# Kernel optimization log

Hardware: AMD Instinct MI355X
Metric: run time of the kernel (lower is better)

Reference implementation:

```python
import jax, jax.numpy as jnp
import numpy as np

B, L, C, R = 2, 1024, 64, 32
RV, DQK, H, NSINK = 32, 64, 8, 4


def setup_inputs() -> dict:
    key = jax.random.key(0)
    ks = jax.random.split(key, 10)
    s_in = 1.0 / np.sqrt(C * R)
    s_r = 1.0 / np.sqrt(R)
    s_rv = 1.0 / np.sqrt(RV)
    return {
        "x": jax.random.normal(ks[0], (B, L, C, R), jnp.float32),
        "Wq": jax.random.normal(ks[1], (C * R, H * DQK), jnp.float32) * s_in,
        "bq": jax.random.normal(ks[2], (H * DQK,), jnp.float32) * s_in,
        "Wk": jax.random.normal(ks[3], (C * R, DQK), jnp.float32) * s_in,
        "bk": jax.random.normal(ks[4], (DQK,), jnp.float32) * s_in,
        "Wv": jax.random.normal(ks[5], (C, R, RV), jnp.float32) * s_r,
        "bv": jax.random.normal(ks[6], (C, RV), jnp.float32) * s_r,
        "Wo": jax.random.normal(ks[7], (C, RV, R), jnp.float32) * s_rv,
        "bo": jax.random.normal(ks[8], (C, R), jnp.float32) * s_rv,
        "sink_q": jax.random.normal(ks[9], (H, NSINK, DQK), jnp.float32),
    }


def reference(x, Wq, bq, Wk, bk, Wv, bv, Wo, bo, sink_q):
    b, l, c, r = x.shape
    h, d_qk = H, DQK
    scale = 1.0 / np.sqrt(d_qk)

    x_flat = x.reshape(b, l, c * r)
    q = (x_flat @ Wq + bq).reshape(b, l, h, d_qk)          # (B,L,H,D)
    k = x_flat @ Wk + bk                                    # (B,L,D) shared MQA key

    # fp32 softmax over time, as in the original
    logits = (jnp.einsum('blhd,bsd->bhls', q, k).astype(jnp.float32) * scale)
    attn = jax.nn.softmax(logits, axis=-1).astype(x.dtype)  # (B,H,L,S)

    # per-channel value projection (B,L,C,RV)
    v = jnp.einsum('blcr,cro->blco', x, Wv) + bv

    # AV with extra channel axis, fused with head-mean (same math as
    # einsum('bhls,bscv->bhlcv').mean(1))
    y = jnp.einsum('bhls,bscv->blcv', attn, v) / h          # (B,L,C,RV)

    # sink-query branch: learned queries attend over time, mean over (H, S)
    logits_s = (jnp.einsum('hsd,bld->bhsl', sink_q, k).astype(jnp.float32) * scale)
    attn_s = jax.nn.softmax(logits_s, axis=-1).astype(x.dtype)  # (B,H,S,L)
    y_sink = jnp.einsum('bhsl,blcv->bcv', attn_s, v) / (h * NSINK)
    y = y + y_sink[:, None]                                 # broadcast over L

    # per-channel output projection + residual
    y = jnp.einsum('blcv,cvr->blcr', y, Wo) + bo
    return x + y
```

## Files before the change

kernel.cpp:

```cpp
#include <hip/hip_runtime.h>
#include <hip/hip_bf16.h>
#include <math.h>


typedef __attribute__((ext_vector_type(8))) short short8;
typedef __attribute__((ext_vector_type(4))) short short4v;
typedef __attribute__((ext_vector_type(4))) float float4v;

__device__ __forceinline__ short f2b(float f) {
    __hip_bfloat16 h = __float2bfloat16(f);
    return __builtin_bit_cast(short, h);
}
__device__ __forceinline__ float b2f(short s) {
    unsigned u = ((unsigned)(unsigned short)s) << 16;
    return __builtin_bit_cast(float, u);
}

__global__ __launch_bounds__(256) void convert_w_kernel(
    const float* __restrict__ Wq, const float* __restrict__ Wk,
    short* __restrict__ Wt)
{
    const int n0 = blockIdx.x * 64;
    const int k0 = blockIdx.y * 64;
    const int tid = threadIdx.x;
    __shared__ float ts[64][65];
    for (int i = tid; i < 4096; i += 256) {
        int kk = i >> 6, nn = i & 63;
        int n = n0 + nn, k = k0 + kk;
        float v = (n < 512) ? Wq[(long)k * 512 + n] : Wk[(long)k * 64 + (n - 512)];
        ts[kk][nn] = v;
    }
    __syncthreads();
    for (int i = tid; i < 4096; i += 256) {
        int nn = i >> 6, kk = i & 63;
        Wt[(long)(n0 + nn) * 2048 + k0 + kk] = f2b(ts[kk][nn]);
    }
}

__global__ __launch_bounds__(256) void vproj_kernel(
    const float* __restrict__ x, const float* __restrict__ Wv,
    const float* __restrict__ bv, short* __restrict__ vt,
    short* __restrict__ xb)
{
    const int c = blockIdx.x;
    const int chunk = blockIdx.y;
    const int b = chunk >> 4;
    const int l0 = (chunk & 15) * 64;
    const int tid = threadIdx.x;
    __shared__ float Wc[32][33];
    __shared__ float xs[64][33];
    for (int i = tid; i < 1024; i += 256)
        Wc[i >> 5][i & 31] = Wv[(c * 32 + (i >> 5)) * 32 + (i & 31)];
    for (int i = tid; i < 2048; i += 256) {
        int s = i >> 5, r = i & 31;
        long gi = ((long)(b << 10) + l0 + s) * 2048 + c * 32 + r;
        float v = x[gi];
        xs[s][r] = v;
        xb[gi] = f2b(v);
    }
    __syncthreads();
    const int s = tid & 63;
    const int og = tid >> 6;
    #pragma unroll
    for (int oi = 0; oi < 8; ++oi) {
        int o = og * 8 + oi;
        float acc = bv[c * 32 + o];
        #pragma unroll
        for (int r = 0; r < 32; ++r) acc += xs[s][r] * Wc[r][o];
        vt[(long)b * (2048 * 1024) + (long)(c * 32 + o) * 1024 + l0 + s] = f2b(acc);
    }
}

__global__ __launch_bounds__(256) void qkproj_kernel(
    const short* __restrict__ xb, const short* __restrict__ Wt,
    float* __restrict__ qkpart)
{
    __shared__ short As[64][72];
    __shared__ short Bs[64][72];

    const int tid = threadIdx.x;
    const int wave = tid >> 6;
    const int lane = tid & 63;
    const int wm = wave >> 1, wn = wave & 1;
    const int m15 = lane & 15;
    const int quad = lane >> 4;
    const int row0 = blockIdx.y * 64;
    const int col0 = blockIdx.x * 64;
    const int kbase = blockIdx.z * 1024;
    float* outz = qkpart + (long)blockIdx.z * 1179648;

    float4v acc[2][2];
    #pragma unroll
    for (int i = 0; i < 2; ++i)
        #pragma unroll
        for (int j = 0; j < 2; ++j)
            #pragma unroll
            for (int r = 0; r < 4; ++r) acc[i][j][r] = 0.f;

    for (int kt = 0; kt < 16; ++kt) {
        int k0 = kbase + kt * 64;
        #pragma unroll
        for (int p = 0; p < 2; ++p) {
            int i = tid + p * 256;
            int m = i >> 3, kq = i & 7;
            *reinterpret_cast<short8*>(&As[m][kq * 8]) =
                *reinterpret_cast<const short8*>(&xb[(long)(row0 + m) * 2048 + k0 + kq * 8]);
        }
        #pragma unroll
        for (int p = 0; p < 2; ++p) {
            int i = tid + p * 256;
            int n = i >> 3, kq = i & 7;
            *reinterpret_cast<short8*>(&Bs[n][kq * 8]) =
                *reinterpret_cast<const short8*>(&Wt[(long)(col0 + n) * 2048 + k0 + kq * 8]);
        }
        __syncthreads();
        #pragma unroll
        for (int ks = 0; ks < 2; ++ks) {
            short8 a[2], b[2];
            #pragma unroll
            for (int t = 0; t < 2; ++t) {
                a[t] = *reinterpret_cast<const short8*>(&As[wm * 32 + t * 16 + m15][ks * 32 + quad * 8]);
                b[t] = *reinterpret_cast<const short8*>(&Bs[wn * 32 + t * 16 + m15][ks * 32 + quad * 8]);
            }
            #pragma unroll
            for (int ti = 0; ti < 2; ++ti)
                #pragma unroll
                for (int tj = 0; tj < 2; ++tj)
                    acc[ti][tj] = __builtin_amdgcn_mfma_f32_16x16x32_bf16(
                        a[ti], b[tj], acc[ti][tj], 0, 0, 0);
        }
        __syncthreads();
    }

    #pragma unroll
    for (int ti = 0; ti < 2; ++ti)
        #pragma unroll
        for (int r = 0; r < 4; ++r) {
            int row = row0 + wm * 32 + ti * 16 + quad * 4 + r;
            #pragma unroll
            for (int tj = 0; tj < 2; ++tj) {
                int col = col0 + wn * 32 + tj * 16 + m15;
                outz[(long)row * 576 + col] = acc[ti][tj][r];
            }
        }
}

__global__ __launch_bounds__(256) void convert_qk_kernel(
    const float* __restrict__ qkpart, const float* __restrict__ bq,
    const float* __restrict__ bk, short* __restrict__ qkb)
{
    int id = blockIdx.x * 256 + threadIdx.x;
    float4 a = reinterpret_cast<const float4*>(qkpart)[id];
    float4 b = reinterpret_cast<const float4*>(qkpart + 1179648)[id];
    int col4 = (id % 144) * 4;
    float4 bias = (col4 < 512)
        ? *reinterpret_cast<const float4*>(&bq[col4])
        : *reinterpret_cast<const float4*>(&bk[col4 - 512]);
    short4v o;
    o[0] = f2b(a.x + b.x + bias.x);
    o[1] = f2b(a.y + b.y + bias.y);
    o[2] = f2b(a.z + b.z + bias.z);
    o[3] = f2b(a.w + b.w + bias.w);
    reinterpret_cast<short4v*>(qkb)[id] = o;
}

__global__ __launch_bounds__(256) void qk_s_kernel(
    const short* __restrict__ qkb, short* __restrict__ S)
{
    const int s0 = blockIdx.x * 64;
    const int l0 = blockIdx.y * 64;
    const int b = blockIdx.z;
    const int tid = threadIdx.x;
    short* Sz = S + ((long)b << 23);

    __shared__ short Qs[64][520];
    __shared__ short Ks[64][72];

    #pragma unroll
    for (int p = 0; p < 16; ++p) {
        int i = tid + p * 256;
        int row = i >> 6, d8 = i & 63;
        *reinterpret_cast<short8*>(&Qs[row][d8 * 8]) =
            *reinterpret_cast<const short8*>(&qkb[(long)((b << 10) + l0 + row) * 576 + d8 * 8]);
    }
    #pragma unroll
    for (int p = 0; p < 2; ++p) {
        int i = tid + p * 256;
        int row = i >> 3, d8 = i & 7;
        *reinterpret_cast<short8*>(&Ks[row][d8 * 8]) =
            *reinterpret_cast<const short8*>(&qkb[(long)((b << 10) + s0 + row) * 576 + 512 + d8 * 8]);
    }
    __syncthreads();

    const int wave = tid >> 6;
    const int lane = tid & 63;
    const int wm = wave >> 1, wn = wave & 1;
    const int m15 = lane & 15;
    const int quad = lane >> 4;

    for (int h = 0; h < 8; ++h) {
        float4v acc[2][2];
        #pragma unroll
        for (int i = 0; i < 2; ++i)
            #pragma unroll
            for (int j = 0; j < 2; ++j)
                #pragma unroll
                for (int r = 0; r < 4; ++r) acc[i][j][r] = 0.f;

        #pragma unroll
        for (int ks = 0; ks < 2; ++ks) {
            short8 a[2], bfr[2];
            #pragma unroll
            for (int t = 0; t < 2; ++t) {
                a[t]   = *reinterpret_cast<const short8*>(
                    &Qs[wm * 32 + t * 16 + m15][h * 64 + ks * 32 + quad * 8]);
                bfr[t] = *reinterpret_cast<const short8*>(
                    &Ks[wn * 32 + t * 16 + m15][ks * 32 + quad * 8]);
            }
            #pragma unroll
            for (int ti = 0; ti < 2; ++ti)
                #pragma unroll
                for (int tj = 0; tj < 2; ++tj)
                    acc[ti][tj] = __builtin_amdgcn_mfma_f32_16x16x32_bf16(
                        a[ti], bfr[tj], acc[ti][tj], 0, 0, 0);
        }

        #pragma unroll
        for (int ti = 0; ti < 2; ++ti)
            #pragma unroll
            for (int r = 0; r < 4; ++r) {
                int l = l0 + wm * 32 + ti * 16 + quad * 4 + r;
                #pragma unroll
                for (int tj = 0; tj < 2; ++tj) {
                    int s = s0 + wn * 32 + tj * 16 + m15;
                    Sz[((long)h << 20) + (l << 10) + s] = f2b(acc[ti][tj][r] * 0.125f);
                }
            }
    }
}

__global__ __launch_bounds__(256) void softmax_avg_kernel(
    const short* __restrict__ S, short* __restrict__ P)
{
    const int l = blockIdx.x;
    const int b = blockIdx.y;
    const int tid = threadIdx.x;
    const int h = tid >> 5, j = tid & 31;
    const short* Sz = S + ((long)b << 23);

    __shared__ float es[8][1032];
    __shared__ float invd[8];

    const short* row = &Sz[((long)h << 20) + (l << 10)];
    float vals[32];
    float pm = -1e30f;
    #pragma unroll
    for (int i = 0; i < 32; ++i) {
        float f = b2f(row[i * 32 + j]);
        vals[i] = f;
        pm = fmaxf(pm, f);
    }
    #pragma unroll
    for (int off = 16; off > 0; off >>= 1) pm = fmaxf(pm, __shfl_down(pm, off, 32));
    pm = __shfl(pm, 0, 32);

    float ps = 0.f;
    #pragma unroll
    for (int i = 0; i < 32; ++i) {
        float e = __expf(vals[i] - pm);
        vals[i] = e;
        ps += e;
    }
    #pragma unroll
    for (int off = 16; off > 0; off >>= 1) ps += __shfl_down(ps, off, 32);
    if (j == 0) invd[h] = 1.f / (8.f * ps);
    __syncthreads();

    const float w = invd[h];
    #pragma unroll
    for (int i = 0; i < 32; ++i) es[h][i * 32 + j] = vals[i] * w;
    __syncthreads();

    for (int s = tid; s < 1024; s += 256) {
        float p = 0.f;
        #pragma unroll
        for (int hh = 0; hh < 8; ++hh) p += es[hh][s];
        P[((long)b << 20) + (l << 10) + s] = f2b(p);
    }
}

__global__ __launch_bounds__(256) void sink_kernel(
    const float* __restrict__ sink_q, const short* __restrict__ qkb,
    float* __restrict__ Psink)
{
    const int z = blockIdx.x;
    const int b = z >> 5;
    const int idx = z & 31;
    const int tid = threadIdx.x;

    __shared__ float sq[64];
    __shared__ float lgl[1024];
    __shared__ float red[4];
    __shared__ float mxs, invs;

    if (tid < 64) sq[tid] = sink_q[idx * 64 + tid];
    __syncthreads();

    float lmax = -1e30f;
    for (int l = tid; l < 1024; l += 256) {
        const short* kp = &qkb[(long)((b << 10) + l) * 576 + 512];
        float acc = 0.f;
        #pragma unroll
        for (int d8 = 0; d8 < 8; ++d8) {
            short8 kv = *reinterpret_cast<const short8*>(&kp[d8 * 8]);
            #pragma unroll
            for (int j = 0; j < 8; ++j) acc += b2f(kv[j]) * sq[d8 * 8 + j];
        }
        acc *= 0.125f;
        lgl[l] = acc;
        lmax = fmaxf(lmax, acc);
    }
    #pragma unroll
    for (int off = 32; off > 0; off >>= 1) lmax = fmaxf(lmax, __shfl_down(lmax, off, 64));
    if ((tid & 63) == 0) red[tid >> 6] = lmax;
    __syncthreads();
    if (tid == 0) mxs = fmaxf(fmaxf(red[0], red[1]), fmaxf(red[2], red[3]));
    __syncthreads();

    const float m = mxs;
    float psum = 0.f;
    for (int l = tid; l < 1024; l += 256) {
        float e = __expf(lgl[l] - m);
        lgl[l] = e;
        psum += e;
    }
    #pragma unroll
    for (int off = 32; off > 0; off >>= 1) psum += __shfl_down(psum, off, 64);
    if ((tid & 63) == 0) red[tid >> 6] = psum;
    __syncthreads();
    if (tid == 0) invs = 1.f / (red[0] + red[1] + red[2] + red[3]);
    __syncthreads();

    const float wgt = invs * (1.f / 32.f);
    for (int l = tid; l < 1024; l += 256)
        atomicAdd(&Psink[(b << 10) + l], lgl[l] * wgt);
}

__global__ __launch_bounds__(256) void sinky_kernel(
    const float* __restrict__ Psink, const short* __restrict__ vt,
    float* __restrict__ Ysink)
{
    const int b = blockIdx.y;
    const int tid = threadIdx.x;
    __shared__ float ps[1024];
    {
        float4 v = reinterpret_cast<const float4*>(&Psink[b << 10])[tid];
        *reinterpret_cast<float4*>(&ps[tid * 4]) = v;
    }
    __syncthreads();
    const int wave = tid >> 6;
    const int lane = tid & 63;
    const int co = blockIdx.x * 4 + wave;
    const short* vp = &vt[((long)b * 2048 + co) * 1024];
    float acc = 0.f;
    #pragma unroll
    for (int t = 0; t < 16; ++t) {
        int l = t * 64 + lane;
        acc += ps[l] * b2f(vp[l]);
    }
    #pragma unroll
    for (int off = 32; off > 0; off >>= 1) acc += __shfl_down(acc, off, 64);
    if (lane == 0) Ysink[(b << 11) + co] = acc;
}

__global__ __launch_bounds__(256) void y_fused_kernel(
    const short* __restrict__ P, const short* __restrict__ vt,
    const float* __restrict__ Ysink, const float* __restrict__ Wo,
    const float* __restrict__ bo, const float* __restrict__ x,
    float* __restrict__ out)
{
    __shared__ short As[128][72];
    __shared__ short Bs[64][72];

    const int tid = threadIdx.x;
    const int b = blockIdx.z;
    const int col0 = blockIdx.x * 64;
    const int row0 = blockIdx.y * 128;
    const short* Pz = P + ((long)b << 20);
    const short* Vz = vt + ((long)b * 2048 * 1024);

    const int wave = tid >> 6;
    const int lane = tid & 63;
    const int wm = wave >> 1, wn = wave & 1;
    const int m15 = lane & 15;
    const int quad = lane >> 4;

    float4v acc[4][2];
    #pragma unroll
    for (int i = 0; i < 4; ++i)
        #pragma unroll
        for (int j = 0; j < 2; ++j)
            #pragma unroll
            for (int r = 0; r < 4; ++r) acc[i][j][r] = 0.f;

    for (int kt = 0; kt < 16; ++kt) {
        int k0 = kt * 64;
        #pragma unroll
        for (int p = 0; p < 4; ++p) {
            int i = tid + p * 256;
            int m = i >> 3, kq = i & 7;
            *reinterpret_cast<short8*>(&As[m][kq * 8]) =
                *reinterpret_cast<const short8*>(&Pz[(long)(row0 + m) * 1024 + k0 + kq * 8]);
        }
        #pragma unroll
        for (int p = 0; p < 2; ++p) {
            int i = tid + p * 256;
            int n = i >> 3, kq = i & 7;
            *reinterpret_cast<short8*>(&Bs[n][kq * 8]) =
                *reinterpret_cast<const short8*>(&Vz[(long)(col0 + n) * 1024 + k0 + kq * 8]);
        }
        __syncthreads();
        #pragma unroll
        for (int ks = 0; ks < 2; ++ks) {
            short8 a[4], bb[2];
            #pragma unroll
            for (int t = 0; t < 4; ++t)
                a[t] = *reinterpret_cast<const short8*>(&As[wm * 64 + t * 16 + m15][ks * 32 + quad * 8]);
            #pragma unroll
            for (int t = 0; t < 2; ++t)
                bb[t] = *reinterpret_cast<const short8*>(&Bs[wn * 32 + t * 16 + m15][ks * 32 + quad * 8]);
            #pragma unroll
            for (int ti = 0; ti < 4; ++ti)
                #pragma unroll
                for (int tj = 0; tj < 2; ++tj)
                    acc[ti][tj] = __builtin_amdgcn_mfma_f32_16x16x32_bf16(
                        a[ti], bb[tj], acc[ti][tj], 0, 0, 0);
        }
        __syncthreads();
    }

    float ysv[2];
    #pragma unroll
    for (int tj = 0; tj < 2; ++tj)
        ysv[tj] = Ysink[(b << 11) + col0 + wn * 32 + tj * 16 + m15];

    #pragma unroll
    for (int ti = 0; ti < 4; ++ti)
        #pragma unroll
        for (int r = 0; r < 4; ++r) {
            int row = wm * 64 + ti * 16 + quad * 4 + r;
            #pragma unroll
            for (int tj = 0; tj < 2; ++tj) {
                int col = wn * 32 + tj * 16 + m15;
                As[row][col] = f2b(acc[ti][tj][r] + ysv[tj]);
            }
        }
    const int c0 = col0 >> 5;
    for (int i = tid; i < 4096; i += 256) {
        int n = i >> 6, k = i & 63;
        short v = 0;
        if ((n >> 5) == (k >> 5))
            v = f2b(Wo[((long)(c0 + (n >> 5)) * 32 + (k & 31)) * 32 + (n & 31)]);
        Bs[n][k] = v;
    }
    __syncthreads();

    float4v acc2[4][2];
    #pragma unroll
    for (int i = 0; i < 4; ++i)
        #pragma unroll
        for (int j = 0; j < 2; ++j)
            #pragma unroll
            for (int r = 0; r < 4; ++r) acc2[i][j][r] = 0.f;

    #pragma unroll
    for (int ks = 0; ks < 2; ++ks) {
        short8 a[4], bb[2];
        #pragma unroll
        for (int t = 0; t < 4; ++t)
            a[t] = *reinterpret_cast<const short8*>(&As[wm * 64 + t * 16 + m15][ks * 32 + quad * 8]);
        #pragma unroll
        for (int t = 0; t < 2; ++t)
            bb[t] = *reinterpret_cast<const short8*>(&Bs[wn * 32 + t * 16 + m15][ks * 32 + quad * 8]);
        #pragma unroll
        for (int ti = 0; ti < 4; ++ti)
            #pragma unroll
            for (int tj = 0; tj < 2; ++tj)
                acc2[ti][tj] = __builtin_amdgcn_mfma_f32_16x16x32_bf16(
                    a[ti], bb[tj], acc2[ti][tj], 0, 0, 0);
    }

    float bov[2];
    #pragma unroll
    for (int tj = 0; tj < 2; ++tj)
        bov[tj] = bo[col0 + wn * 32 + tj * 16 + m15];

    #pragma unroll
    for (int ti = 0; ti < 4; ++ti)
        #pragma unroll
        for (int r = 0; r < 4; ++r) {
            int row = (b << 10) + row0 + wm * 64 + ti * 16 + quad * 4 + r;
            #pragma unroll
            for (int tj = 0; tj < 2; ++tj) {
                int col = col0 + wn * 32 + tj * 16 + m15;
                long oi = (long)row * 2048 + col;
                out[oi] = x[oi] + bov[tj] + acc2[ti][tj][r];
            }
        }
}

extern "C" void kernel_launch(void* const* d_in, const int* in_sizes, int n_in,
                              void* d_out, int out_size, void* d_ws, size_t ws_size,
                              hipStream_t stream)
{
    const float* x  = (const float*)d_in[0];
    const float* Wq = (const float*)d_in[1];
    const float* bq = (const float*)d_in[2];
    const float* Wk = (const float*)d_in[3];
    const float* bk = (const float*)d_in[4];
    const float* Wv = (const float*)d_in[5];
    const float* bv = (const float*)d_in[6];
    const float* Wo = (const float*)d_in[7];
    const float* bo = (const float*)d_in[8];
    const float* sq = (const float*)d_in[9];
    float* out = (float*)d_out;

    float* ws = (float*)d_ws;
    float* qkpart = ws;
    short* qkb    = (short*)(ws + 2359296);
    short* P      = (short*)(ws + 2949120);
    float* Psink  = ws + 3997696;
    short* vt     = (short*)(ws + 3999744);
    float* Ysink  = ws + 6096896;
    float* region = ws + 6100992;
    short* xb     = (short*)region;
    short* Wt     = (short*)(region + 2097152);
    short* Sb     = (short*)region;

    dim3 blk(256);

    convert_w_kernel<<<dim3(9, 32), blk, 0, stream>>>(Wq, Wk, Wt);
    vproj_kernel<<<dim3(64, 32), blk, 0, stream>>>(x, Wv, bv, vt, xb);
    qkproj_kernel<<<dim3(9, 32, 2), blk, 0, stream>>>(xb, Wt, qkpart);
    convert_qk_kernel<<<dim3(1152), blk, 0, stream>>>(qkpart, bq, bk, qkb);
    qk_s_kernel<<<dim3(16, 16, 2), blk, 0, stream>>>(qkb, Sb);
    softmax_avg_kernel<<<dim3(1024, 2), blk, 0, stream>>>(Sb, P);
    hipMemsetAsync(Psink, 0, 2048 * sizeof(float), stream);
    sink_kernel<<<dim3(64), blk, 0, stream>>>(sq, qkb, Psink);
    sinky_kernel<<<dim3(512, 2), blk, 0, stream>>>(Psink, vt, Ysink);
    y_fused_kernel<<<dim3(32, 8, 2), blk, 0, stream>>>(
        P, vt, Ysink, Wo, bo, x, out);
}
```

Before: 194.2 us.

## Replace materialized logits and softmax pass with two-pass recompute of exp sums

Stops writing the full bf16 logits tensor (B*H*L*L) to global memory and reading it back in a separate softmax kernel. The first kernel computes QK^T per tile and atomically accumulates per-row exp sums. The second recomputes QK^T and writes the head-averaged normalized probabilities directly. It skips max subtraction, which relies on logits being small enough not to overflow exp, and it doubles the QK matmul work plus adds atomics.

```diff
diff --git a/kernel.cpp b/kernel.cpp
--- a/kernel.cpp
+++ b/kernel.cpp
@@ -164,25 +164,18 @@
     reinterpret_cast<short4v*>(qkb)[id] = o;
 }
 
-__global__ __launch_bounds__(256) void qk_s_kernel(
-    const short* __restrict__ qkb, short* __restrict__ S)
+__global__ __launch_bounds__(256) void attn_sum_kernel(
+    const short* __restrict__ qkb, float* __restrict__ sums)
 {
     const int s0 = blockIdx.x * 64;
     const int l0 = blockIdx.y * 64;
     const int b = blockIdx.z;
     const int tid = threadIdx.x;
-    short* Sz = S + ((long)b << 23);
-
-    __shared__ short Qs[64][520];
+
+    __shared__ short Qh[64][72];
     __shared__ short Ks[64][72];
-
-    #pragma unroll
-    for (int p = 0; p < 16; ++p) {
-        int i = tid + p * 256;
-        int row = i >> 6, d8 = i & 63;
-        *reinterpret_cast<short8*>(&Qs[row][d8 * 8]) =
-            *reinterpret_cast<const short8*>(&qkb[(long)((b << 10) + l0 + row) * 576 + d8 * 8]);
-    }
+    __shared__ float ssum[8][64];
+
     #pragma unroll
     for (int p = 0; p < 2; ++p) {
         int i = tid + p * 256;
@@ -190,6 +183,11 @@
         *reinterpret_cast<short8*>(&Ks[row][d8 * 8]) =
             *reinterpret_cast<const short8*>(&qkb[(long)((b << 10) + s0 + row) * 576 + 512 + d8 * 8]);
     }
+    {
+        int h = tid >> 5, c = tid & 31;
+        ssum[h][c] = 0.f;
+        ssum[h][32 + c] = 0.f;
+    }
     __syncthreads();
 
     const int wave = tid >> 6;
@@ -199,6 +197,15 @@
     const int quad = lane >> 4;
 
     for (int h = 0; h < 8; ++h) {
+        #pragma unroll
+        for (int p = 0; p < 2; ++p) {
+            int i = tid + p * 256;
+            int row = i >> 3, d8 = i & 7;
+            *reinterpret_cast<short8*>(&Qh[row][d8 * 8]) =
+                *reinterpret_cast<const short8*>(&qkb[(long)((b << 10) + l0 + row) * 576 + h * 64 + d8 * 8]);
+        }
+        __syncthreads();
+
         float4v acc[2][2];
         #pragma unroll
         for (int i = 0; i < 2; ++i)
@@ -212,10 +219,8 @@
             short8 a[2], bfr[2];
             #pragma unroll
             for (int t = 0; t < 2; ++t) {
-                a[t]   = *reinterpret_cast<const short8*>(
-                    &Qs[wm * 32 + t * 16 + m15][h * 64 + ks * 32 + quad * 8]);
-                bfr[t] = *reinterpret_cast<const short8*>(
-                    &Ks[wn * 32 + t * 16 + m15][ks * 32 + quad * 8]);
+                a[t]   = *reinterpret_cast<const short8*>(&Qh[wm * 32 + t * 16 + m15][ks * 32 + quad * 8]);
+                bfr[t] = *reinterpret_cast<const short8*>(&Ks[wn * 32 + t * 16 + m15][ks * 32 + quad * 8]);
             }
             #pragma unroll
             for (int ti = 0; ti < 2; ++ti)
@@ -226,66 +231,136 @@
         }
 
         #pragma unroll
+        for (int ti = 0; ti < 2; ++ti) {
+            float rs[4];
+            #pragma unroll
+            for (int r = 0; r < 4; ++r)
+                rs[r] = __expf(acc[ti][0][r] * 0.125f) + __expf(acc[ti][1][r] * 0.125f);
+            #pragma unroll
+            for (int off = 8; off > 0; off >>= 1)
+                #pragma unroll
+                for (int r = 0; r < 4; ++r)
+                    rs[r] += __shfl_down(rs[r], off, 16);
+            if (m15 == 0) {
+                #pragma unroll
+                for (int r = 0; r < 4; ++r)
+                    atomicAdd(&ssum[h][wm * 32 + ti * 16 + quad * 4 + r], rs[r]);
+            }
+        }
+        __syncthreads();
+    }
+
+    {
+        int h = tid >> 5, c = tid & 31;
+        atomicAdd(&sums[((long)(b * 8 + h) << 10) + l0 + c], ssum[h][c]);
+        atomicAdd(&sums[((long)(b * 8 + h) << 10) + l0 + 32 + c], ssum[h][32 + c]);
+    }
+}
+
+__global__ __launch_bounds__(256) void attn_p_kernel(
+    const short* __restrict__ qkb, const float* __restrict__ sums,
+    short* __restrict__ P)
+{
+    const int s0 = blockIdx.x * 64;
+    const int l0 = blockIdx.y * 64;
+    const int b = blockIdx.z;
+    const int tid = threadIdx.x;
+
+    __shared__ short Qh[64][72];
+    __shared__ short Ks[64][72];
+    __shared__ short Rp[64][72];
+    __shared__ float warr[8][64];
+
+    #pragma unroll
+    for (int p = 0; p < 2; ++p) {
+        int i = tid + p * 256;
+        int row = i >> 3, d8 = i & 7;
+        *reinterpret_cast<short8*>(&Ks[row][d8 * 8]) =
+            *reinterpret_cast<const short8*>(&qkb[(long)((b << 10) + s0 + row) * 576 + 512 + d8 * 8]);
+    }
+    {
+        int h = tid >> 5, c = tid & 31;
+        warr[h][c]      = 1.f / (8.f * sums[((long)(b * 8 + h) << 10) + l0 + c]);
+        warr[h][32 + c] = 1.f / (8.f * sums[((long)(b * 8 + h) << 10) + l0 + 32 + c]);
+    }
+    __syncthreads();
+
+    const int wave = tid >> 6;
+    const int lane = tid & 63;
+    const int wm = wave >> 1, wn = wave & 1;
+    const int m15 = lane & 15;
+    const int quad = lane >> 4;
+
+    float pacc[2][2][4];
+    #pragma unroll
+    for (int i = 0; i < 2; ++i)
+        #pragma unroll
+        for (int j = 0; j < 2; ++j)
+            #pragma unroll
+            for (int r = 0; r < 4; ++r) pacc[i][j][r] = 0.f;
+
+    for (int h = 0; h < 8; ++h) {
+        #pragma unroll
+        for (int p = 0; p < 2; ++p) {
+            int i = tid + p * 256;
+            int row = i >> 3, d8 = i & 7;
+            *reinterpret_cast<short8*>(&Qh[row][d8 * 8]) =
+                *reinterpret_cast<const short8*>(&qkb[(long)((b << 10) + l0 + row) * 576 + h * 64 + d8 * 8]);
+        }
+        __syncthreads();
+
+        float4v acc[2][2];
+        #pragma unroll
+        for (int i = 0; i < 2; ++i)
+            #pragma unroll
+            for (int j = 0; j < 2; ++j)
+                #pragma unroll
+                for (int r = 0; r < 4; ++r) acc[i][j][r] = 0.f;
+
+        #pragma unroll
+        for (int ks = 0; ks < 2; ++ks) {
+            short8 a[2], bfr[2];
+            #pragma unroll
+            for (int t = 0; t < 2; ++t) {
+                a[t]   = *reinterpret_cast<const short8*>(&Qh[wm * 32 + t * 16 + m15][ks * 32 + quad * 8]);
+                bfr[t] = *reinterpret_cast<const short8*>(&Ks[wn * 32 + t * 16 + m15][ks * 32 + quad * 8]);
+            }
+            #pragma unroll
+            for (int ti = 0; ti < 2; ++ti)
+                #pragma unroll
+                for (int tj = 0; tj < 2; ++tj)
+                    acc[ti][tj] = __builtin_amdgcn_mfma_f32_16x16x32_bf16(
+                        a[ti], bfr[tj], acc[ti][tj], 0, 0, 0);
+        }
+
+        #pragma unroll
         for (int ti = 0; ti < 2; ++ti)
             #pragma unroll
             for (int r = 0; r < 4; ++r) {
-                int l = l0 + wm * 32 + ti * 16 + quad * 4 + r;
-                #pragma unroll
-                for (int tj = 0; tj < 2; ++tj) {
-                    int s = s0 + wn * 32 + tj * 16 + m15;
-                    Sz[((long)h << 20) + (l << 10) + s] = f2b(acc[ti][tj][r] * 0.125f);
-                }
-            }
-    }
-}
-
-__global__ __launch_bounds__(256) void softmax_avg_kernel(
-    const short* __restrict__ S, short* __restrict__ P)
-{
-    const int l = blockIdx.x;
-    const int b = blockIdx.y;
-    const int tid = threadIdx.x;
-    const int h = tid >> 5, j = tid & 31;
-    const short* Sz = S + ((long)b << 23);
-
-    __shared__ float es[8][1032];
-    __shared__ float invd[8];
-
-    const short* row = &Sz[((long)h << 20) + (l << 10)];
-    float vals[32];
-    float pm = -1e30f;
-    #pragma unroll
-    for (int i = 0; i < 32; ++i) {
-        float f = b2f(row[i * 32 + j]);
-        vals[i] = f;
-        pm = fmaxf(pm, f);
-    }
-    #pragma unroll
-    for (int off = 16; off > 0; off >>= 1) pm = fmaxf(pm, __shfl_down(pm, off, 32));
-    pm = __shfl(pm, 0, 32);
-
-    float ps = 0.f;
-    #pragma unroll
-    for (int i = 0; i < 32; ++i) {
-        float e = __expf(vals[i] - pm);
-        vals[i] = e;
-        ps += e;
-    }
-    #pragma unroll
-    for (int off = 16; off > 0; off >>= 1) ps += __shfl_down(ps, off, 32);
-    if (j == 0) invd[h] = 1.f / (8.f * ps);
-    __syncthreads();
-
-    const float w = invd[h];
-    #pragma unroll
-    for (int i = 0; i < 32; ++i) es[h][i * 32 + j] = vals[i] * w;
-    __syncthreads();
-
-    for (int s = tid; s < 1024; s += 256) {
-        float p = 0.f;
-        #pragma unroll
-        for (int hh = 0; hh < 8; ++hh) p += es[hh][s];
-        P[((long)b << 20) + (l << 10) + s] = f2b(p);
+                float w = warr[h][wm * 32 + ti * 16 + quad * 4 + r];
+                #pragma unroll
+                for (int tj = 0; tj < 2; ++tj)
+                    pacc[ti][tj][r] += w * __expf(acc[ti][tj][r] * 0.125f);
+            }
+        __syncthreads();
+    }
+
+    #pragma unroll
+    for (int ti = 0; ti < 2; ++ti)
+        #pragma unroll
+        for (int r = 0; r < 4; ++r) {
+            int row = wm * 32 + ti * 16 + quad * 4 + r;
+            #pragma unroll
+            for (int tj = 0; tj < 2; ++tj)
+                Rp[row][wn * 32 + tj * 16 + m15] = f2b(pacc[ti][tj][r]);
+        }
+    __syncthreads();
+    #pragma unroll
+    for (int p = 0; p < 2; ++p) {
+        int i = tid + p * 256;
+        int row = i >> 3, c8 = i & 7;
+        *reinterpret_cast<short8*>(&P[((long)b << 20) + ((long)(l0 + row) << 10) + s0 + c8 * 8]) =
+            *reinterpret_cast<const short8*>(&Rp[row][c8 * 8]);
     }
 }
 
@@ -532,20 +607,21 @@
     float* Psink  = ws + 3997696;
     short* vt     = (short*)(ws + 3999744);
     float* Ysink  = ws + 6096896;
-    float* region = ws + 6100992;
+    float* sums   = ws + 6100992;
+    float* region = ws + 6117376;
     short* xb     = (short*)region;
     short* Wt     = (short*)(region + 2097152);
-    short* Sb     = (short*)region;
 
     dim3 blk(256);
 
+    hipMemsetAsync(sums, 0, 16384 * sizeof(float), stream);
+    hipMemsetAsync(Psink, 0, 2048 * sizeof(float), stream);
     convert_w_kernel<<<dim3(9, 32), blk, 0, stream>>>(Wq, Wk, Wt);
     vproj_kernel<<<dim3(64, 32), blk, 0, stream>>>(x, Wv, bv, vt, xb);
     qkproj_kernel<<<dim3(9, 32, 2), blk, 0, stream>>>(xb, Wt, qkpart);
     convert_qk_kernel<<<dim3(1152), blk, 0, stream>>>(qkpart, bq, bk, qkb);
-    qk_s_kernel<<<dim3(16, 16, 2), blk, 0, stream>>>(qkb, Sb);
-    softmax_avg_kernel<<<dim3(1024, 2), blk, 0, stream>>>(Sb, P);
-    hipMemsetAsync(Psink, 0, 2048 * sizeof(float), stream);
+    attn_sum_kernel<<<dim3(16, 16, 2), blk, 0, stream>>>(qkb, sums);
+    attn_p_kernel<<<dim3(16, 16, 2), blk, 0, stream>>>(qkb, sums, P);
     sink_kernel<<<dim3(64), blk, 0, stream>>>(sq, qkb, Psink);
     sinky_kernel<<<dim3(512, 2), blk, 0, stream>>>(Psink, vt, Ysink);
     y_fused_kernel<<<dim3(32, 8, 2), blk, 0, stream>>>(
```

Measured after the change: 201.3 us. 1.04x slower.
